# Performance work log

Hardware: AMD Instinct MI355X
Metric: run time of the kernel (lower is better)

Reference implementation:

```python
import jax, jax.numpy as jnp
import numpy as np

HEADS = 16
CHANNELS = 1024
CPH = CHANNELS // HEADS
B, S = 2, 2048


def setup_inputs() -> dict:
    key = jax.random.key(0)
    ks = jax.random.split(key, 10)
    scale = 1.0 / np.sqrt(CHANNELS)
    inp = {
        "Q": jax.random.normal(ks[0], (B, CHANNELS, S), dtype=jnp.float32),
        "K": jax.random.normal(ks[1], (B, CHANNELS, S), dtype=jnp.float32),
        "V": jax.random.normal(ks[2], (B, CHANNELS, S), dtype=jnp.float32),
        "mask": jax.random.randint(ks[3], (B, S, S), 0, 2).astype(bool),
        # nn.Linear params: weight [out, in], bias [out]
        "Wq": jax.random.uniform(ks[4], (CHANNELS, CHANNELS), jnp.float32, -scale, scale),
        "bq": jax.random.uniform(ks[5], (CHANNELS,), jnp.float32, -scale, scale),
        "Wk": jax.random.uniform(ks[6], (CHANNELS, CHANNELS), jnp.float32, -scale, scale),
        "bk": jax.random.uniform(ks[7], (CHANNELS,), jnp.float32, -scale, scale),
        "Wv": jax.random.uniform(ks[8], (CHANNELS, CHANNELS), jnp.float32, -scale, scale),
        "bv": jax.random.uniform(ks[9], (CHANNELS,), jnp.float32, -scale, scale),
    }
    return inp


def reference(Q, K, V, mask, Wq, bq, Wk, bk, Wv, bv):
    b = Q.shape[0]
    # inputs are [B, C, S] -> transpose to [B, S, C], project, split heads
    def proj(x, W, bias):
        y = jnp.einsum('bcs,oc->bso', x, W) + bias  # [B, S, C]
        return y.reshape(b, -1, HEADS, CPH).transpose(0, 2, 1, 3)  # [B, H, S, cph]

    q = proj(Q, Wq, bq)
    k = proj(K, Wk, bk)
    v = proj(V, Wv, bv)
    scores = jnp.einsum('bhqd,bhkd->bhqk', q, k) / np.sqrt(CPH).astype(np.float32)
    scores = jnp.where(mask[:, None, :, :], jnp.float32(-1e9), scores)
    attn = jax.nn.softmax(scores, axis=-1)
    ctx = jnp.einsum('bhqk,bhkd->bhqd', attn, v)  # [B, H, S, cph]
    return ctx.transpose(0, 2, 1, 3).reshape(b, -1, HEADS * CPH)
```

## Files before the change

### kernel.cpp

```cpp
#include <hip/hip_runtime.h>
#include <hip/hip_bf16.h>
#include <stdint.h>

#define NH   16
#define CPH  64
#define CH   1024
#define BATCH 2
#define SEQ  2048

typedef __bf16    bf16x8 __attribute__((ext_vector_type(8)));
typedef float     f32x4  __attribute__((ext_vector_type(4)));
typedef uint16_t  u16x8  __attribute__((ext_vector_type(8)));

static __device__ inline uint16_t f2bf(float f) {
  union { float f; unsigned u; } v; v.f = f;
  unsigned r = (v.u + 0x7FFFu + ((v.u >> 16) & 1u)) >> 16;
  return (uint16_t)r;
}

static __device__ inline float fast_exp2(float x) {
  float r;
  asm("v_exp_f32 %0, %1" : "=v"(r) : "v"(x));
  return r;
}

__global__ void k_detect(const unsigned int* __restrict__ m, int* __restrict__ flag) {
  unsigned v = m[threadIdx.x & 63];
  unsigned long long ok = __ballot(v <= 1u);
  if (threadIdx.x == 0) *flag = (ok == ~0ull) ? 1 : 0;
}

__global__ void k_packmask(const void* __restrict__ mask, const int* __restrict__ flag,
                           unsigned long long* __restrict__ pm) {
  int row  = blockIdx.x * 4 + (threadIdx.x >> 6);
  int lane = threadIdx.x & 63;
  unsigned long long* prow = pm + (size_t)row * (SEQ / 64);
  if (*flag != 0) {
    const int* m = (const int*)mask + (size_t)row * SEQ;
    for (int wi = 0; wi < SEQ / 64; wi++) {
      unsigned long long bits = __ballot(m[wi * 64 + lane] != 0);
      if (lane == 0) prow[wi] = bits;
    }
  } else {
    const unsigned char* m = (const unsigned char*)mask + (size_t)row * SEQ;
    for (int wi = 0; wi < SEQ / 64; wi++) {
      unsigned long long bits = __ballot(m[wi * 64 + lane] != 0);
      if (lane == 0) prow[wi] = bits;
    }
  }
}

__global__ void k_castw(const float* __restrict__ W0, const float* __restrict__ W1,
                        const float* __restrict__ W2, uint16_t* __restrict__ dst) {
  const float* W = blockIdx.z == 0 ? W0 : (blockIdx.z == 1 ? W1 : W2);
  uint16_t* o = dst + (size_t)blockIdx.z * (CH * CH);
  int idx = (blockIdx.x * 256 + threadIdx.x) * 4;
  float4 w = *(const float4*)(W + idx);
  o[idx + 0] = f2bf(w.x); o[idx + 1] = f2bf(w.y);
  o[idx + 2] = f2bf(w.z); o[idx + 3] = f2bf(w.w);
}

__global__ void k_transpose(const float* __restrict__ Q, const float* __restrict__ K,
                            const float* __restrict__ V, uint16_t* __restrict__ XT) {
  int z = blockIdx.z;
  int p = z % 3, b = z / 3;
  const float* X = (p == 0 ? Q : (p == 1 ? K : V)) + (size_t)b * CH * SEQ;
  uint16_t* T = XT + ((size_t)p * BATCH + b) * SEQ * CH;
  __shared__ float t[32][33];
  int tx = threadIdx.x, ty = threadIdx.y;
  int s0 = blockIdx.x * 32, c0 = blockIdx.y * 32;
#pragma unroll
  for (int i = 0; i < 4; i++)
    t[ty + 8 * i][tx] = X[(size_t)(c0 + ty + 8 * i) * SEQ + s0 + tx];
  __syncthreads();
#pragma unroll
  for (int i = 0; i < 4; i++)
    T[(size_t)(s0 + ty + 8 * i) * CH + c0 + tx] = f2bf(t[tx][ty + 8 * i]);
}

__global__ __launch_bounds__(256)
void k_proj(const uint16_t* __restrict__ XT, const uint16_t* __restrict__ Wbf,
            const float* __restrict__ bq, const float* __restrict__ bk,
            const float* __restrict__ bv,
            uint16_t* __restrict__ qbuf, uint16_t* __restrict__ kbuf,
            uint16_t* __restrict__ vtbuf) {
  int z = blockIdx.z, p = z % 3, b = z / 3;
  const uint16_t* X = XT + ((size_t)p * BATCH + b) * SEQ * CH;
  const uint16_t* W = Wbf + (size_t)p * CH * CH;
  const float* bias = p == 0 ? bq : (p == 1 ? bk : bv);
  int s0 = blockIdx.x * 128, o0 = blockIdx.y * 128;

  __shared__ __align__(16) uint16_t Al[128 * 64];
  __shared__ __align__(16) uint16_t Bl[128 * 64];

  int tid = threadIdx.x, lane = tid & 63, w = tid >> 6;
  int g = lane >> 4, li = lane & 15;
  int wm = w >> 1, wn = w & 1;
  int lr = lane >> 3, lc = lane & 7;

  f32x4 acc[4][4] = {};

  for (int c0 = 0; c0 < CH; c0 += 64) {
    const uint16_t* gA = W + (size_t)(o0 + w * 32) * CH + c0;
    const uint16_t* gB = X + (size_t)(s0 + w * 32) * CH + c0;
#pragma unroll
    for (int i = 0; i < 4; i++) {
      __builtin_amdgcn_global_load_lds(
          (const __attribute__((address_space(1))) void*)(gA + (size_t)(i * 8 + lr) * CH + lc * 8),
          (__attribute__((address_space(3))) void*)(Al + (w * 32 + i * 8) * 64),
          16, 0, 0);
      __builtin_amdgcn_global_load_lds(
          (const __attribute__((address_space(1))) void*)(gB + (size_t)(i * 8 + lr) * CH + lc * 8),
          (__attribute__((address_space(3))) void*)(Bl + (w * 32 + i * 8) * 64),
          16, 0, 0);
    }
    __syncthreads();

#pragma unroll
    for (int ks = 0; ks < 2; ks++) {
      bf16x8 af[4], bfr[4];
#pragma unroll
      for (int mt = 0; mt < 4; mt++)
        af[mt] = *(const bf16x8*)&Al[(wm * 64 + mt * 16 + li) * 64 + ks * 32 + g * 8];
#pragma unroll
      for (int nt = 0; nt < 4; nt++)
        bfr[nt] = *(const bf16x8*)&Bl[(wn * 64 + nt * 16 + li) * 64 + ks * 32 + g * 8];
#pragma unroll
      for (int mt = 0; mt < 4; mt++)
#pragma unroll
        for (int nt = 0; nt < 4; nt++)
          acc[mt][nt] = __builtin_amdgcn_mfma_f32_16x16x32_bf16(af[mt], bfr[nt], acc[mt][nt], 0, 0, 0);
    }
    __syncthreads();
  }

  int h = (o0 >> 6) + wm;
  float scale = (p == 0) ? 0.18033688011112042f : 1.0f;
  size_t bh = (size_t)b * NH + h;
#pragma unroll
  for (int mt = 0; mt < 4; mt++) {
#pragma unroll
    for (int r = 0; r < 4; r++) {
      int dd = mt * 16 + g * 4 + r;
      float bi = bias[o0 + wm * 64 + dd];
#pragma unroll
      for (int nt = 0; nt < 4; nt++) {
        int s = s0 + wn * 64 + nt * 16 + li;
        float v = (acc[mt][nt][r] + bi) * scale;
        if (p == 2)
          vtbuf[(bh * CPH + dd) * SEQ + s] = f2bf(v);
        else {
          uint16_t* dst = (p == 0) ? qbuf : kbuf;
          dst[(bh * SEQ + s) * CPH + dd] = f2bf(v);
        }
      }
    }
  }
}

__global__ __launch_bounds__(256, 4)
void k_attn(const uint16_t* __restrict__ qbuf, const uint16_t* __restrict__ kbuf,
            const uint16_t* __restrict__ vtbuf,
            const unsigned long long* __restrict__ pm, float* __restrict__ out) {
  int bid = blockIdx.x;
  int logical = (bid & 7) * 128 + (bid >> 3);
  int bx = logical & 31, bhh = logical >> 5;
  int b = bhh >> 4, h = bhh & 15;
  int q0 = bx * 64;
  const uint16_t* qb = qbuf + ((size_t)b * NH + h) * SEQ * CPH;
  const uint16_t* kb = kbuf + ((size_t)b * NH + h) * SEQ * CPH;
  const uint16_t* vt = vtbuf + ((size_t)b * NH + h) * CPH * SEQ;
  const unsigned long long* pmb = pm + (size_t)b * SEQ * (SEQ / 64);
  int tid = threadIdx.x, lane = tid & 63, w = tid >> 6;
  int g = lane >> 4, li = lane & 15;
  int qw = q0 + w * 16;
  __shared__ uint16_t Kl[64][80];
  __shared__ uint16_t Vl[64][80];
  __shared__ uint16_t Pl[4][16][76];

  bf16x8 aq[2];
#pragma unroll
  for (int ks = 0; ks < 2; ks++)
    aq[ks] = *(const bf16x8*)&qb[(size_t)(qw + li) * CPH + ks * 32 + g * 8];

  u16x8 oneu = {0x3F80, 0x3F80, 0x3F80, 0x3F80, 0x3F80, 0x3F80, 0x3F80, 0x3F80};
  bf16x8 ones = *(bf16x8*)&oneu;

  f32x4 octx[4] = {{0,0,0,0},{0,0,0,0},{0,0,0,0},{0,0,0,0}};
  f32x4 sacc = {0,0,0,0};

  int r8 = tid >> 3, ch = tid & 7;

  for (int kv0 = 0; kv0 < SEQ; kv0 += 64) {
    int kw = kv0 >> 6;
#pragma unroll
    for (int i = 0; i < 64; i += 32) {
      *(u16x8*)&Kl[r8 + i][ch * 8] =
          *(const u16x8*)&kb[(size_t)(kv0 + r8 + i) * CPH + ch * 8];
      *(u16x8*)&Vl[r8 + i][ch * 8] =
          *(const u16x8*)&vt[(size_t)(r8 + i) * SEQ + kv0 + ch * 8];
    }
    unsigned long long mw[4];
#pragma unroll
    for (int r = 0; r < 4; r++)
      mw[r] = pmb[(size_t)(qw + g * 4 + r) * (SEQ / 64) + kw];
    __syncthreads();

    f32x4 sc[4] = {{0,0,0,0},{0,0,0,0},{0,0,0,0},{0,0,0,0}};
#pragma unroll
    for (int ks = 0; ks < 2; ks++)
#pragma unroll
      for (int nt = 0; nt < 4; nt++) {
        bf16x8 kf = *(const bf16x8*)&Kl[nt * 16 + li][ks * 32 + g * 8];
        sc[nt] = __builtin_amdgcn_mfma_f32_16x16x32_bf16(aq[ks], kf, sc[nt], 0, 0, 0);
      }

#pragma unroll
    for (int nt = 0; nt < 4; nt++)
#pragma unroll
      for (int r = 0; r < 4; r++) {
        float e = fast_exp2(sc[nt][r]);
        unsigned bit = (unsigned)(mw[r] >> (nt * 16 + li)) & 1u;
        float pv = bit ? 0.0f : e;
        Pl[w][g * 4 + r][nt * 16 + li] = f2bf(pv);
      }

#pragma unroll
    for (int ks = 0; ks < 2; ks++) {
      bf16x8 ap = *(const bf16x8*)&Pl[w][li][ks * 32 + g * 8];
      sacc = __builtin_amdgcn_mfma_f32_16x16x32_bf16(ap, ones, sacc, 0, 0, 0);
#pragma unroll
      for (int nt = 0; nt < 4; nt++) {
        bf16x8 vf = *(const bf16x8*)&Vl[nt * 16 + li][ks * 32 + g * 8];
        octx[nt] = __builtin_amdgcn_mfma_f32_16x16x32_bf16(ap, vf, octx[nt], 0, 0, 0);
      }
    }
    __syncthreads();
  }

#pragma unroll
  for (int r = 0; r < 4; r++) {
    float inv = 1.0f / sacc[r];
    int qrow = qw + g * 4 + r;
#pragma unroll
    for (int nt = 0; nt < 4; nt++) {
      int d = nt * 16 + li;
      out[((size_t)b * SEQ + qrow) * CH + h * CPH + d] = octx[nt][r] * inv;
    }
  }
}

extern "C" void kernel_launch(void* const* d_in, const int* in_sizes, int n_in,
                              void* d_out, int out_size, void* d_ws, size_t ws_size,
                              hipStream_t stream) {
  (void)in_sizes; (void)n_in; (void)out_size; (void)ws_size;
  const float* Q  = (const float*)d_in[0];
  const float* K  = (const float*)d_in[1];
  const float* V  = (const float*)d_in[2];
  const void*  Mk = d_in[3];
  const float* Wq = (const float*)d_in[4];
  const float* bq = (const float*)d_in[5];
  const float* Wk = (const float*)d_in[6];
  const float* bk = (const float*)d_in[7];
  const float* Wv = (const float*)d_in[8];
  const float* bv = (const float*)d_in[9];
  char* ws = (char*)d_ws;

  int*      flag  = (int*)ws;
  uint16_t* XT    = (uint16_t*)(ws + 256);
  uint16_t* Wbf   = (uint16_t*)(ws + 256 + 3ull * BATCH * SEQ * CH * 2);
  uint16_t* qbuf  = (uint16_t*)((char*)Wbf + 3ull * CH * CH * 2);
  uint16_t* kbuf  = qbuf + (size_t)BATCH * NH * SEQ * CPH;
  uint16_t* vtbuf = kbuf + (size_t)BATCH * NH * SEQ * CPH;
  unsigned long long* pmask = (unsigned long long*)XT;
  float* out = (float*)d_out;

  hipLaunchKernelGGL(k_detect, dim3(1), dim3(64), 0, stream,
                     (const unsigned int*)Mk, flag);
  hipLaunchKernelGGL(k_castw, dim3(CH * CH / 1024, 1, 3), dim3(256), 0, stream,
                     Wq, Wk, Wv, Wbf);
  hipLaunchKernelGGL(k_transpose, dim3(SEQ / 32, CH / 32, 6), dim3(32, 8), 0, stream,
                     Q, K, V, XT);
  hipLaunchKernelGGL(k_proj, dim3(SEQ / 128, CH / 128, 6), dim3(256), 0, stream,
                     XT, Wbf, bq, bk, bv, qbuf, kbuf, vtbuf);
  hipLaunchKernelGGL(k_packmask, dim3(BATCH * SEQ / 4), dim3(256), 0, stream,
                     Mk, flag, pmask);
  hipLaunchKernelGGL(k_attn, dim3(1024), dim3(256), 0, stream,
                     qbuf, kbuf, vtbuf, pmask, out);
}
```

Before: 156.6 us.

## Process two 16-row query fragments per wave to double K/V tile reuse

Each attention block now covers 128 query rows instead of 64, with every wave handling two 16-row fragments that share the same K and V fragments loaded from LDS. The grid is halved to 512 blocks and the block-index swizzle is adjusted to match. The aim is to halve the global-to-LDS K/V traffic per query and amortise LDS fragment reads over twice the MFMA work. In exchange each thread needs more accumulator registers, there are fewer blocks to fill the GPU, and an extra __syncthreads is added between writing and reading P in each iteration.

Measured after the change: 212.1 us. 1.35x slower.

```diff
diff --git a/kernel.cpp b/kernel.cpp
--- a/kernel.cpp
+++ b/kernel.cpp
@@ -163,31 +163,34 @@
             const uint16_t* __restrict__ vtbuf,
             const unsigned long long* __restrict__ pm, float* __restrict__ out) {
   int bid = blockIdx.x;
-  int logical = (bid & 7) * 128 + (bid >> 3);
-  int bx = logical & 31, bhh = logical >> 5;
+  int logical = (bid & 7) * 64 + (bid >> 3);
+  int bx = logical & 15, bhh = logical >> 4;
   int b = bhh >> 4, h = bhh & 15;
-  int q0 = bx * 64;
+  int q0 = bx * 128;
   const uint16_t* qb = qbuf + ((size_t)b * NH + h) * SEQ * CPH;
   const uint16_t* kb = kbuf + ((size_t)b * NH + h) * SEQ * CPH;
   const uint16_t* vt = vtbuf + ((size_t)b * NH + h) * CPH * SEQ;
   const unsigned long long* pmb = pm + (size_t)b * SEQ * (SEQ / 64);
   int tid = threadIdx.x, lane = tid & 63, w = tid >> 6;
   int g = lane >> 4, li = lane & 15;
-  int qw = q0 + w * 16;
+  int qw = q0 + w * 32;
   __shared__ uint16_t Kl[64][80];
   __shared__ uint16_t Vl[64][80];
-  __shared__ uint16_t Pl[4][16][76];
-
-  bf16x8 aq[2];
-#pragma unroll
-  for (int ks = 0; ks < 2; ks++)
-    aq[ks] = *(const bf16x8*)&qb[(size_t)(qw + li) * CPH + ks * 32 + g * 8];
+  __shared__ uint16_t Pl[4][32][76];
+
+  bf16x8 aq[2][2];
+#pragma unroll
+  for (int f = 0; f < 2; f++)
+#pragma unroll
+    for (int ks = 0; ks < 2; ks++)
+      aq[f][ks] = *(const bf16x8*)&qb[(size_t)(qw + f * 16 + li) * CPH + ks * 32 + g * 8];
 
   u16x8 oneu = {0x3F80, 0x3F80, 0x3F80, 0x3F80, 0x3F80, 0x3F80, 0x3F80, 0x3F80};
   bf16x8 ones = *(bf16x8*)&oneu;
 
-  f32x4 octx[4] = {{0,0,0,0},{0,0,0,0},{0,0,0,0},{0,0,0,0}};
-  f32x4 sacc = {0,0,0,0};
+  f32x4 octx[2][4] = {{{0,0,0,0},{0,0,0,0},{0,0,0,0},{0,0,0,0}},
+                      {{0,0,0,0},{0,0,0,0},{0,0,0,0},{0,0,0,0}}};
+  f32x4 sacc[2] = {{0,0,0,0},{0,0,0,0}};
 
   int r8 = tid >> 3, ch = tid & 7;
 
@@ -200,54 +203,67 @@
       *(u16x8*)&Vl[r8 + i][ch * 8] =
           *(const u16x8*)&vt[(size_t)(r8 + i) * SEQ + kv0 + ch * 8];
     }
-    unsigned long long mw[4];
-#pragma unroll
-    for (int r = 0; r < 4; r++)
-      mw[r] = pmb[(size_t)(qw + g * 4 + r) * (SEQ / 64) + kw];
-    __syncthreads();
-
-    f32x4 sc[4] = {{0,0,0,0},{0,0,0,0},{0,0,0,0},{0,0,0,0}};
+    unsigned long long mw[2][4];
+#pragma unroll
+    for (int f = 0; f < 2; f++)
+#pragma unroll
+      for (int r = 0; r < 4; r++)
+        mw[f][r] = pmb[(size_t)(qw + f * 16 + g * 4 + r) * (SEQ / 64) + kw];
+    __syncthreads();
+
+    f32x4 sc[2][4] = {{{0,0,0,0},{0,0,0,0},{0,0,0,0},{0,0,0,0}},
+                      {{0,0,0,0},{0,0,0,0},{0,0,0,0},{0,0,0,0}}};
 #pragma unroll
     for (int ks = 0; ks < 2; ks++)
 #pragma unroll
       for (int nt = 0; nt < 4; nt++) {
         bf16x8 kf = *(const bf16x8*)&Kl[nt * 16 + li][ks * 32 + g * 8];
-        sc[nt] = __builtin_amdgcn_mfma_f32_16x16x32_bf16(aq[ks], kf, sc[nt], 0, 0, 0);
+        sc[0][nt] = __builtin_amdgcn_mfma_f32_16x16x32_bf16(aq[0][ks], kf, sc[0][nt], 0, 0, 0);
+        sc[1][nt] = __builtin_amdgcn_mfma_f32_16x16x32_bf16(aq[1][ks], kf, sc[1][nt], 0, 0, 0);
       }
 
 #pragma unroll
-    for (int nt = 0; nt < 4; nt++)
-#pragma unroll
-      for (int r = 0; r < 4; r++) {
-        float e = fast_exp2(sc[nt][r]);
-        unsigned bit = (unsigned)(mw[r] >> (nt * 16 + li)) & 1u;
-        float pv = bit ? 0.0f : e;
-        Pl[w][g * 4 + r][nt * 16 + li] = f2bf(pv);
+    for (int f = 0; f < 2; f++)
+#pragma unroll
+      for (int nt = 0; nt < 4; nt++)
+#pragma unroll
+        for (int r = 0; r < 4; r++) {
+          float e = fast_exp2(sc[f][nt][r]);
+          unsigned bit = (unsigned)(mw[f][r] >> (nt * 16 + li)) & 1u;
+          float p = bit ? 0.0f : e;
+          Pl[w][f * 16 + g * 4 + r][nt * 16 + li] = f2bf(p);
+        }
+
+    __syncthreads();
+
+#pragma unroll
+    for (int ks = 0; ks < 2; ks++) {
+      bf16x8 ap0 = *(const bf16x8*)&Pl[w][li][ks * 32 + g * 8];
+      bf16x8 ap1 = *(const bf16x8*)&Pl[w][16 + li][ks * 32 + g * 8];
+      sacc[0] = __builtin_amdgcn_mfma_f32_16x16x32_bf16(ap0, ones, sacc[0], 0, 0, 0);
+      sacc[1] = __builtin_amdgcn_mfma_f32_16x16x32_bf16(ap1, ones, sacc[1], 0, 0, 0);
+#pragma unroll
+      for (int nt = 0; nt < 4; nt++) {
+        bf16x8 vf16 = *(const bf16x8*)&Vl[nt * 16 + li][ks * 32 + g * 8];
+        octx[0][nt] = __builtin_amdgcn_mfma_f32_16x16x32_bf16(ap0, vf16, octx[0][nt], 0, 0, 0);
+        octx[1][nt] = __builtin_amdgcn_mfma_f32_16x16x32_bf16(ap1, vf16, octx[1][nt], 0, 0, 0);
       }
-
-#pragma unroll
-    for (int ks = 0; ks < 2; ks++) {
-      bf16x8 ap = *(const bf16x8*)&Pl[w][li][ks * 32 + g * 8];
-      sacc = __builtin_amdgcn_mfma_f32_16x16x32_bf16(ap, ones, sacc, 0, 0, 0);
+    }
+    __syncthreads();
+  }
+
+#pragma unroll
+  for (int f = 0; f < 2; f++)
+#pragma unroll
+    for (int r = 0; r < 4; r++) {
+      float inv = 1.0f / sacc[f][r];
+      int qrow = qw + f * 16 + g * 4 + r;
 #pragma unroll
       for (int nt = 0; nt < 4; nt++) {
-        bf16x8 vf = *(const bf16x8*)&Vl[nt * 16 + li][ks * 32 + g * 8];
-        octx[nt] = __builtin_amdgcn_mfma_f32_16x16x32_bf16(ap, vf, octx[nt], 0, 0, 0);
+        int d = nt * 16 + li;
+        out[((size_t)b * SEQ + qrow) * CH + h * CPH + d] = octx[f][nt][r] * inv;
       }
     }
-    __syncthreads();
-  }
-
-#pragma unroll
-  for (int r = 0; r < 4; r++) {
-    float inv = 1.0f / sacc[r];
-    int qrow = qw + g * 4 + r;
-#pragma unroll
-    for (int nt = 0; nt < 4; nt++) {
-      int d = nt * 16 + li;
-      out[((size_t)b * SEQ + qrow) * CH + h * CPH + d] = octx[nt][r] * inv;
-    }
-  }
 }
 
 extern "C" void kernel_launch(void* const* d_in, const int* in_sizes, int n_in,
@@ -285,6 +301,6 @@
                      XT, Wbf, bq, bk, bv, qbuf, kbuf, vtbuf);
   hipLaunchKernelGGL(k_packmask, dim3(BATCH * SEQ / 4), dim3(256), 0, stream,
                      Mk, flag, pmask);
-  hipLaunchKernelGGL(k_attn, dim3(1024), dim3(256), 0, stream,
+  hipLaunchKernelGGL(k_attn, dim3(512), dim3(256), 0, stream,
                      qbuf, kbuf, vtbuf, pmask, out);
 }
```
